# Kernel optimization log

Hardware: AMD Instinct MI355X
Metric: run time of the kernel (lower is better)

Reference implementation:

```python
import jax, jax.numpy as jnp
import numpy as np

N, IN_F, OUT_F = 4096, 4096, 4096
THRESH = 0.05


def setup_inputs() -> dict:
    key = jax.random.key(0)
    k_x, k_w = jax.random.split(key)
    last_out = jax.random.normal(k_x, (N, IN_F), dtype=jnp.float32)
    # learned weight buffer, [out_features, in_features] like torch Linear
    weight = jax.random.normal(k_w, (OUT_F, IN_F), dtype=jnp.float32) * (1.0 / np.sqrt(IN_F))
    threshold = jnp.float32(THRESH)
    return {"last_out": last_out, "weight": weight, "threshold": threshold}


def reference(last_out, weight, threshold):
    # rtp_linear: runtime threshold pruning — activations with |x| <= threshold
    # are skipped (treated as zero) in the matmul. Bias buffer is unused
    # (dead code in the original forward).
    x = jnp.where(jnp.abs(last_out) > threshold, last_out, 0.0)
    # y[n, o] = sum_i x[n, i] * W[o, i]
    return jnp.einsum("ni,oi->no", x, weight)
```

## Files before the change

### kernel.cpp

```cpp
#include <hip/hip_runtime.h>
#include <hip/hip_bf16.h>

#define M_DIM 4096
#define N_DIM 4096
#define K_DIM 4096

typedef __attribute__((ext_vector_type(8))) __bf16 bf16x8;
typedef __attribute__((ext_vector_type(8))) short short8;
typedef __attribute__((ext_vector_type(8))) unsigned short ushort8;
typedef __attribute__((ext_vector_type(4))) float f32x4;

__device__ __forceinline__ void gload_lds16(const void* g, void* l) {
    __builtin_amdgcn_global_load_lds(
        (const __attribute__((address_space(1))) void*)g,
        (__attribute__((address_space(3))) void*)l,
        16, 0, 0);
}

__device__ __forceinline__ bf16x8 ld8(const unsigned short* p) {
    short8 r = *reinterpret_cast<const short8*>(p);
    return __builtin_bit_cast(bf16x8, r);
}

__global__ void prune_cvt2(const float* __restrict__ x,
                           const float* __restrict__ w,
                           unsigned short* __restrict__ xb,
                           unsigned short* __restrict__ wb,
                           const float* __restrict__ thrp, int n8) {
    const float thr = thrp[0];
    const int stride = gridDim.x * blockDim.x;
    const int total = 2 * n8;
    for (int idx = blockIdx.x * blockDim.x + threadIdx.x; idx < total; idx += stride) {
        const bool isx = idx < n8;
        const int j = isx ? idx : idx - n8;
        const float* src = isx ? x : w;
        unsigned short* dst = isx ? xb : wb;
        const float te = isx ? thr : -1.0f;
        const float4* p = reinterpret_cast<const float4*>(src) + 2 * (size_t)j;
        float4 v0 = p[0];
        float4 v1 = p[1];
        float v[8] = {v0.x, v0.y, v0.z, v0.w, v1.x, v1.y, v1.z, v1.w};
        ushort8 o;
#pragma unroll
        for (int e = 0; e < 8; ++e) {
            float f = v[e];
            f = (fabsf(f) > te) ? f : 0.0f;
            __hip_bfloat16 hh = __float2bfloat16(f);
            o[e] = *reinterpret_cast<unsigned short*>(&hh);
        }
        *reinterpret_cast<ushort8*>(dst + 8 * (size_t)j) = o;
    }
}

__global__ __launch_bounds__(512, 2) void gemm_8phase(
        const unsigned short* __restrict__ A,
        const unsigned short* __restrict__ B,
        float* __restrict__ C) {
    __shared__ __align__(16) unsigned short lds[65536];

    const int tid  = threadIdx.x;
    const int lane = tid & 63;
    const int wid  = tid >> 6;
    const int wr   = wid >> 2;
    const int wc   = wid & 3;

    const int bid = blockIdx.x;
    const int swz = (bid & 7) * 32 + (bid >> 3);
    const int bm = (swz >> 4) * 256;
    const int bn = (swz & 15) * 256;

    const int g  = tid & 255;
    const int ah = tid >> 8;
    const int arow = bm + ah * 128 + (g >> 3);
    const int acol = 8 * ((g & 7) ^ ((g >> 3) & 7));
    const unsigned short* Asrc = A + (size_t)arow * K_DIM + acol;
    const int AdstE = ah * 8192 + g * 8;

    const int h = lane + 64 * wr;
    const int brow = bn + wc * 64 + (h >> 3);
    const int bcol = 8 * ((h & 7) ^ ((h >> 3) & 7));
    const unsigned short* Bsrc = B + (size_t)brow * K_DIM + bcol;
    const int BdstE = wc * 4096 + h * 8;

#define SA(dstb, j, kg) gload_lds16(Asrc + (size_t)(32*(j))*K_DIM + (kg), (dstb) + AdstE + 2048*(j))
#define SB(dstb, j, kg) gload_lds16(Bsrc + (size_t)(16*(j))*K_DIM + (kg), (dstb) + BdstE + 1024*(j))

    const int fr  = lane & 15;
    const int kq4 = lane >> 4;
    const int rowOffA = (wr * 128 + fr) * 64;
    const int rowOffB = (wc * 64 + fr) * 64;
    const int sk0 = 8 * ((kq4    ) ^ (fr & 7));
    const int sk1 = 8 * ((kq4 + 4) ^ (fr & 7));

    f32x4 acc[8][4] = {};

    bf16x8 bfr[4][2];
#define MFMA16(q, A00, A10, A01, A11)                                                              \
    __builtin_amdgcn_s_setprio(1);                                                                 \
    _Pragma("unroll")                                                                              \
    for (int n = 0; n < 4; ++n) {                                                                  \
        acc[2*(q)][n]   = __builtin_amdgcn_mfma_f32_16x16x32_bf16(A00, bfr[n][0], acc[2*(q)][n], 0, 0, 0);   \
        acc[2*(q)+1][n] = __builtin_amdgcn_mfma_f32_16x16x32_bf16(A10, bfr[n][0], acc[2*(q)+1][n], 0, 0, 0); \
    }                                                                                              \
    _Pragma("unroll")                                                                              \
    for (int n = 0; n < 4; ++n) {                                                                  \
        acc[2*(q)][n]   = __builtin_amdgcn_mfma_f32_16x16x32_bf16(A01, bfr[n][1], acc[2*(q)][n], 0, 0, 0);   \
        acc[2*(q)+1][n] = __builtin_amdgcn_mfma_f32_16x16x32_bf16(A11, bfr[n][1], acc[2*(q)+1][n], 0, 0, 0); \
    }                                                                                              \
    __builtin_amdgcn_s_setprio(0);

#define TILE_BODY(Ab, Bb, AbN, BbN, kn)                                                            \
    {                                                                                              \
                             \
        _Pragma("unroll")                                                                          \
        for (int n = 0; n < 4; ++n) {                                                              \
            bfr[n][0] = ld8((Bb) + rowOffB + n * 1024 + sk0);                                      \
            bfr[n][1] = ld8((Bb) + rowOffB + n * 1024 + sk1);                                      \
        }                                                                                          \
        bf16x8 q00 = ld8((Ab) + rowOffA + 2 * 1024 + sk0);                                         \
        bf16x8 q10 = ld8((Ab) + rowOffA + 3 * 1024 + sk0);                                         \
        bf16x8 q01 = ld8((Ab) + rowOffA + 2 * 1024 + sk1);                                         \
        bf16x8 q11 = ld8((Ab) + rowOffA + 3 * 1024 + sk1);                                         \
        SB((BbN), 0, (kn)); SB((BbN), 1, (kn)); SB((BbN), 2, (kn)); SB((BbN), 3, (kn));            \
        SA((AbN), 0, (kn)); SA((AbN), 1, (kn)); SA((AbN), 2, (kn)); SA((AbN), 3, (kn));            \
        MFMA16(0, p00, p10, p01, p11);                                                             \
                                                           \
        bf16x8 r00 = ld8((Ab) + rowOffA + 4 * 1024 + sk0);                                         \
        bf16x8 r10 = ld8((Ab) + rowOffA + 5 * 1024 + sk0);                                         \
        bf16x8 r01 = ld8((Ab) + rowOffA + 4 * 1024 + sk1);                                         \
        bf16x8 r11 = ld8((Ab) + rowOffA + 5 * 1024 + sk1);                                         \
        MFMA16(1, q00, q10, q01, q11);                                                             \
                                        \
        bf16x8 s00 = ld8((Ab) + rowOffA + 6 * 1024 + sk0);                                         \
        bf16x8 s10 = ld8((Ab) + rowOffA + 7 * 1024 + sk0);                                         \
        bf16x8 s01 = ld8((Ab) + rowOffA + 6 * 1024 + sk1);                                         \
        bf16x8 s11 = ld8((Ab) + rowOffA + 7 * 1024 + sk1);                                         \
        MFMA16(2, r00, r10, r01, r11);                                                             \
        asm volatile("s_waitcnt lgkmcnt(0) vmcnt(0)" ::: "memory");                                \
        asm volatile("s_barrier" ::: "memory");                                                    \
                                       \
        p00 = ld8((AbN) + rowOffA + 0 * 1024 + sk0);                                               \
        p10 = ld8((AbN) + rowOffA + 1 * 1024 + sk0);                                               \
        p01 = ld8((AbN) + rowOffA + 0 * 1024 + sk1);                                               \
        p11 = ld8((AbN) + rowOffA + 1 * 1024 + sk1);                                               \
        MFMA16(3, s00, s10, s01, s11);                                                             \
    }

    unsigned short* A0 = lds;
    unsigned short* A1 = lds + 16384;
    unsigned short* B0 = lds + 32768;
    unsigned short* B1 = lds + 49152;

    SB(B0, 0, 0); SB(B0, 1, 0); SB(B0, 2, 0); SB(B0, 3, 0);
    SA(A0, 0, 0); SA(A0, 1, 0); SA(A0, 2, 0); SA(A0, 3, 0);
    asm volatile("s_waitcnt vmcnt(0)" ::: "memory");
    asm volatile("s_barrier" ::: "memory");

    bf16x8 p00 = ld8(A0 + rowOffA + 0 * 1024 + sk0);
    bf16x8 p10 = ld8(A0 + rowOffA + 1 * 1024 + sk0);
    bf16x8 p01 = ld8(A0 + rowOffA + 0 * 1024 + sk1);
    bf16x8 p11 = ld8(A0 + rowOffA + 1 * 1024 + sk1);

    for (int t = 0; t < 64; t += 2) {
        const int kn0 = (t + 1) * 64;
        const int kn1 = (t + 2 < 64 ? t + 2 : 63) * 64;
        TILE_BODY(A0, B0, A1, B1, kn0);
        TILE_BODY(A1, B1, A0, B0, kn1);
    }

    asm volatile("s_waitcnt vmcnt(0)" ::: "memory");

    const int crow = bm + wr * 128 + kq4 * 4;
    const int ccol = bn + wc * 64 + fr;
#pragma unroll
    for (int m = 0; m < 8; ++m)
#pragma unroll
        for (int n = 0; n < 4; ++n)
#pragma unroll
            for (int j = 0; j < 4; ++j)
                C[(size_t)(crow + m * 16 + j) * N_DIM + ccol + n * 16] = acc[m][n][j];
}

__global__ void gemm_f32_fallback(const float* __restrict__ A,
                                  const float* __restrict__ B,
                                  float* __restrict__ C,
                                  const float* __restrict__ thrp) {
    __shared__ float As[32][33];
    __shared__ float Bs[32][33];
    const float thr = thrp[0];
    const int tx = threadIdx.x, ty = threadIdx.y;
    const int row = blockIdx.y * 32 + ty;
    float acc = 0.0f;
    for (int k0 = 0; k0 < K_DIM; k0 += 32) {
        float a = A[(size_t)row * K_DIM + k0 + tx];
        As[ty][tx] = (fabsf(a) > thr) ? a : 0.0f;
        Bs[ty][tx] = B[(size_t)(blockIdx.x * 32 + ty) * K_DIM + k0 + tx];
        __syncthreads();
#pragma unroll 8
        for (int kk = 0; kk < 32; ++kk)
            acc += As[ty][kk] * Bs[tx][kk];
        __syncthreads();
    }
    C[(size_t)row * N_DIM + blockIdx.x * 32 + tx] = acc;
}

extern "C" void kernel_launch(void* const* d_in, const int* in_sizes, int n_in,
                              void* d_out, int out_size, void* d_ws, size_t ws_size,
                              hipStream_t stream) {
    const float* x    = (const float*)d_in[0];
    const float* w    = (const float*)d_in[1];
    const float* thrp = (const float*)d_in[2];
    float* out = (float*)d_out;

    const size_t elems = (size_t)M_DIM * K_DIM;
    if (ws_size >= 2 * elems * sizeof(unsigned short)) {
        unsigned short* Ab = (unsigned short*)d_ws;
        unsigned short* Bb = Ab + elems;
        const int n8 = (int)(elems / 8);
        prune_cvt2<<<2048, 256, 0, stream>>>(x, w, Ab, Bb, thrp, n8);
        gemm_8phase<<<dim3(256), dim3(512), 0, stream>>>(Ab, Bb, out);
    } else {
        dim3 grid(N_DIM / 32, M_DIM / 32), blk(32, 32);
        gemm_f32_fallback<<<grid, blk, 0, stream>>>(x, w, out, thrp);
    }
}
```

Before: 142.6 us.

## Load B fragments directly from global into registers, halve LDS usage

The B operand no longer goes through LDS. Each wave loads its B fragments straight from global memory into registers one tile ahead, and only A stays double-buffered in LDS, which halves shared memory. The block-to-tile mapping is also changed so each XCD handles two columns of B tiles, improving L2 reuse of B. The cost is uncoalesced 16-byte global loads per lane, higher register pressure, and global latency exposed inside the MFMA schedule.

New measurement: 215.8 us. +51.3%, slower.

```diff
diff --git a/kernel.cpp b/kernel.cpp
--- a/kernel.cpp
+++ b/kernel.cpp
@@ -52,11 +52,11 @@
     }
 }
 
-__global__ __launch_bounds__(512, 2) void gemm_8phase(
+__global__ __launch_bounds__(512, 2) void gemm_bgl(
         const unsigned short* __restrict__ A,
         const unsigned short* __restrict__ B,
         float* __restrict__ C) {
-    __shared__ __align__(16) unsigned short lds[65536];
+    __shared__ __align__(16) unsigned short lds[32768];
 
     const int tid  = threadIdx.x;
     const int lane = tid & 63;
@@ -64,10 +64,10 @@
     const int wr   = wid >> 2;
     const int wc   = wid & 3;
 
-    const int bid = blockIdx.x;
-    const int swz = (bid & 7) * 32 + (bid >> 3);
-    const int bm = (swz >> 4) * 256;
-    const int bn = (swz & 15) * 256;
+    const int xcd = blockIdx.x & 7;
+    const int idx = blockIdx.x >> 3;
+    const int bn  = (xcd * 2 + (idx >> 4)) * 256;
+    const int bm  = (idx & 15) * 256;
 
     const int g  = tid & 255;
     const int ah = tid >> 8;
@@ -76,96 +76,97 @@
     const unsigned short* Asrc = A + (size_t)arow * K_DIM + acol;
     const int AdstE = ah * 8192 + g * 8;
 
-    const int h = lane + 64 * wr;
-    const int brow = bn + wc * 64 + (h >> 3);
-    const int bcol = 8 * ((h & 7) ^ ((h >> 3) & 7));
-    const unsigned short* Bsrc = B + (size_t)brow * K_DIM + bcol;
-    const int BdstE = wc * 4096 + h * 8;
-
 #define SA(dstb, j, kg) gload_lds16(Asrc + (size_t)(32*(j))*K_DIM + (kg), (dstb) + AdstE + 2048*(j))
-#define SB(dstb, j, kg) gload_lds16(Bsrc + (size_t)(16*(j))*K_DIM + (kg), (dstb) + BdstE + 1024*(j))
 
     const int fr  = lane & 15;
     const int kq4 = lane >> 4;
     const int rowOffA = (wr * 128 + fr) * 64;
-    const int rowOffB = (wc * 64 + fr) * 64;
     const int sk0 = 8 * ((kq4    ) ^ (fr & 7));
     const int sk1 = 8 * ((kq4 + 4) ^ (fr & 7));
 
+    const unsigned short* bp0 = B + (size_t)(bn + wc * 64 +  0 + fr) * K_DIM + kq4 * 8;
+    const unsigned short* bp1 = bp0 + (size_t)16 * K_DIM;
+    const unsigned short* bp2 = bp0 + (size_t)32 * K_DIM;
+    const unsigned short* bp3 = bp0 + (size_t)48 * K_DIM;
+
     f32x4 acc[8][4] = {};
-
-    bf16x8 bfr[4][2];
-#define MFMA16(q, A00, A10, A01, A11)                                                              \
+    bf16x8 aA0, aA1, aA2, aA3, aB0, aB1, aB2, aB3;
+    bf16x8 e0[4], e1[4], o0[4], o1[4];
+
+#define PH_MFMA(q, S0, S1, S2, S3, T)                                                              \
     __builtin_amdgcn_s_setprio(1);                                                                 \
-    _Pragma("unroll")                                                                              \
-    for (int n = 0; n < 4; ++n) {                                                                  \
-        acc[2*(q)][n]   = __builtin_amdgcn_mfma_f32_16x16x32_bf16(A00, bfr[n][0], acc[2*(q)][n], 0, 0, 0);   \
-        acc[2*(q)+1][n] = __builtin_amdgcn_mfma_f32_16x16x32_bf16(A10, bfr[n][0], acc[2*(q)+1][n], 0, 0, 0); \
-    }                                                                                              \
-    _Pragma("unroll")                                                                              \
-    for (int n = 0; n < 4; ++n) {                                                                  \
-        acc[2*(q)][n]   = __builtin_amdgcn_mfma_f32_16x16x32_bf16(A01, bfr[n][1], acc[2*(q)][n], 0, 0, 0);   \
-        acc[2*(q)+1][n] = __builtin_amdgcn_mfma_f32_16x16x32_bf16(A11, bfr[n][1], acc[2*(q)+1][n], 0, 0, 0); \
+    {                                                                                              \
+        const bf16x8 Av_[4] = {S0, S1, S2, S3};                                                    \
+        _Pragma("unroll")                                                                          \
+        for (int i_ = 0; i_ < 4; ++i_)                                                             \
+            _Pragma("unroll")                                                                      \
+            for (int n_ = 0; n_ < 4; ++n_)                                                         \
+                acc[4*(q)+i_][n_] = __builtin_amdgcn_mfma_f32_16x16x32_bf16(                       \
+                    Av_[i_], T[n_], acc[4*(q)+i_][n_], 0, 0, 0);                                   \
     }                                                                                              \
     __builtin_amdgcn_s_setprio(0);
 
-#define TILE_BODY(Ab, Bb, AbN, BbN, kn)                                                            \
+#define TILE_BODY(Ab, AbN, BC0, BC1, BN0, kc, kna, knb)                                            \
     {                                                                                              \
-                             \
-        _Pragma("unroll")                                                                          \
-        for (int n = 0; n < 4; ++n) {                                                              \
-            bfr[n][0] = ld8((Bb) + rowOffB + n * 1024 + sk0);                                      \
-            bfr[n][1] = ld8((Bb) + rowOffB + n * 1024 + sk1);                                      \
-        }                                                                                          \
-        bf16x8 q00 = ld8((Ab) + rowOffA + 2 * 1024 + sk0);                                         \
-        bf16x8 q10 = ld8((Ab) + rowOffA + 3 * 1024 + sk0);                                         \
-        bf16x8 q01 = ld8((Ab) + rowOffA + 2 * 1024 + sk1);                                         \
-        bf16x8 q11 = ld8((Ab) + rowOffA + 3 * 1024 + sk1);                                         \
-        SB((BbN), 0, (kn)); SB((BbN), 1, (kn)); SB((BbN), 2, (kn)); SB((BbN), 3, (kn));            \
-        SA((AbN), 0, (kn)); SA((AbN), 1, (kn)); SA((AbN), 2, (kn)); SA((AbN), 3, (kn));            \
-        MFMA16(0, p00, p10, p01, p11);                                                             \
-                                                           \
-        bf16x8 r00 = ld8((Ab) + rowOffA + 4 * 1024 + sk0);                                         \
-        bf16x8 r10 = ld8((Ab) + rowOffA + 5 * 1024 + sk0);                                         \
-        bf16x8 r01 = ld8((Ab) + rowOffA + 4 * 1024 + sk1);                                         \
-        bf16x8 r11 = ld8((Ab) + rowOffA + 5 * 1024 + sk1);                                         \
-        MFMA16(1, q00, q10, q01, q11);                                                             \
-                                        \
-        bf16x8 s00 = ld8((Ab) + rowOffA + 6 * 1024 + sk0);                                         \
-        bf16x8 s10 = ld8((Ab) + rowOffA + 7 * 1024 + sk0);                                         \
-        bf16x8 s01 = ld8((Ab) + rowOffA + 6 * 1024 + sk1);                                         \
-        bf16x8 s11 = ld8((Ab) + rowOffA + 7 * 1024 + sk1);                                         \
-        MFMA16(2, r00, r10, r01, r11);                                                             \
+                                \
+        BC1[0] = ld8(bp0 + (kc) + 32);                                                             \
+        BC1[1] = ld8(bp1 + (kc) + 32);                                                             \
+        BC1[2] = ld8(bp2 + (kc) + 32);                                                             \
+        BC1[3] = ld8(bp3 + (kc) + 32);                                                             \
+        aB0 = ld8((Ab) + rowOffA + 4 * 1024 + sk0);                                                \
+        aB1 = ld8((Ab) + rowOffA + 5 * 1024 + sk0);                                                \
+        aB2 = ld8((Ab) + rowOffA + 6 * 1024 + sk0);                                                \
+        aB3 = ld8((Ab) + rowOffA + 7 * 1024 + sk0);                                                \
+        SA((AbN), 0, (kna)); SA((AbN), 1, (kna)); SA((AbN), 2, (kna)); SA((AbN), 3, (kna));        \
+        PH_MFMA(0, aA0, aA1, aA2, aA3, BC0);                                                       \
+                                                 \
+        aA0 = ld8((Ab) + rowOffA + 0 * 1024 + sk1);                                                \
+        aA1 = ld8((Ab) + rowOffA + 1 * 1024 + sk1);                                                \
+        aA2 = ld8((Ab) + rowOffA + 2 * 1024 + sk1);                                                \
+        aA3 = ld8((Ab) + rowOffA + 3 * 1024 + sk1);                                                \
+        PH_MFMA(1, aB0, aB1, aB2, aB3, BC0);                                                       \
+                                    \
+        aB0 = ld8((Ab) + rowOffA + 4 * 1024 + sk1);                                                \
+        aB1 = ld8((Ab) + rowOffA + 5 * 1024 + sk1);                                                \
+        aB2 = ld8((Ab) + rowOffA + 6 * 1024 + sk1);                                                \
+        aB3 = ld8((Ab) + rowOffA + 7 * 1024 + sk1);                                                \
+        PH_MFMA(0, aA0, aA1, aA2, aA3, BC1);                                                       \
         asm volatile("s_waitcnt lgkmcnt(0) vmcnt(0)" ::: "memory");                                \
         asm volatile("s_barrier" ::: "memory");                                                    \
-                                       \
-        p00 = ld8((AbN) + rowOffA + 0 * 1024 + sk0);                                               \
-        p10 = ld8((AbN) + rowOffA + 1 * 1024 + sk0);                                               \
-        p01 = ld8((AbN) + rowOffA + 0 * 1024 + sk1);                                               \
-        p11 = ld8((AbN) + rowOffA + 1 * 1024 + sk1);                                               \
-        MFMA16(3, s00, s10, s01, s11);                                                             \
+                 \
+        BN0[0] = ld8(bp0 + (knb));                                                                 \
+        BN0[1] = ld8(bp1 + (knb));                                                                 \
+        BN0[2] = ld8(bp2 + (knb));                                                                 \
+        BN0[3] = ld8(bp3 + (knb));                                                                 \
+        aA0 = ld8((AbN) + rowOffA + 0 * 1024 + sk0);                                               \
+        aA1 = ld8((AbN) + rowOffA + 1 * 1024 + sk0);                                               \
+        aA2 = ld8((AbN) + rowOffA + 2 * 1024 + sk0);                                               \
+        aA3 = ld8((AbN) + rowOffA + 3 * 1024 + sk0);                                               \
+        PH_MFMA(1, aB0, aB1, aB2, aB3, BC1);                                                       \
     }
 
     unsigned short* A0 = lds;
     unsigned short* A1 = lds + 16384;
-    unsigned short* B0 = lds + 32768;
-    unsigned short* B1 = lds + 49152;
-
-    SB(B0, 0, 0); SB(B0, 1, 0); SB(B0, 2, 0); SB(B0, 3, 0);
+
     SA(A0, 0, 0); SA(A0, 1, 0); SA(A0, 2, 0); SA(A0, 3, 0);
+    e0[0] = ld8(bp0); e0[1] = ld8(bp1); e0[2] = ld8(bp2); e0[3] = ld8(bp3);
     asm volatile("s_waitcnt vmcnt(0)" ::: "memory");
     asm volatile("s_barrier" ::: "memory");
 
-    bf16x8 p00 = ld8(A0 + rowOffA + 0 * 1024 + sk0);
-    bf16x8 p10 = ld8(A0 + rowOffA + 1 * 1024 + sk0);
-    bf16x8 p01 = ld8(A0 + rowOffA + 0 * 1024 + sk1);
-    bf16x8 p11 = ld8(A0 + rowOffA + 1 * 1024 + sk1);
+    aA0 = ld8(A0 + rowOffA + 0 * 1024 + sk0);
+    aA1 = ld8(A0 + rowOffA + 1 * 1024 + sk0);
+    aA2 = ld8(A0 + rowOffA + 2 * 1024 + sk0);
+    aA3 = ld8(A0 + rowOffA + 3 * 1024 + sk0);
 
     for (int t = 0; t < 64; t += 2) {
-        const int kn0 = (t + 1) * 64;
-        const int kn1 = (t + 2 < 64 ? t + 2 : 63) * 64;
-        TILE_BODY(A0, B0, A1, B1, kn0);
-        TILE_BODY(A1, B1, A0, B0, kn1);
+        const int kc0 = t * 64;
+        const int kc1 = (t + 1) * 64;
+        const int kna0 = (t + 1) * 64;
+        const int kna1 = (t + 2 < 64 ? t + 2 : 63) * 64;
+        const int knb0 = kc1;
+        const int knb1 = kna1;
+        TILE_BODY(A0, A1, e0, e1, o0, kc0, kna0, knb0);
+        TILE_BODY(A1, A0, o0, o1, e0, kc1, kna1, knb1);
     }
 
     asm volatile("s_waitcnt vmcnt(0)" ::: "memory");
@@ -218,7 +219,7 @@
         unsigned short* Bb = Ab + elems;
         const int n8 = (int)(elems / 8);
         prune_cvt2<<<2048, 256, 0, stream>>>(x, w, Ab, Bb, thrp, n8);
-        gemm_8phase<<<dim3(256), dim3(512), 0, stream>>>(Ab, Bb, out);
+        gemm_bgl<<<dim3(256), dim3(512), 0, stream>>>(Ab, Bb, out);
     } else {
         dim3 grid(N_DIM / 32, M_DIM / 32), blk(32, 32);
         gemm_f32_fallback<<<grid, blk, 0, stream>>>(x, w, out, thrp);
```
